# Optimization experiments

Hardware: AMD Instinct MI355X
Metric: run time of the kernel (lower is better)

## Reference

```python
import jax, jax.numpy as jnp
import numpy as np
import math

N_HEADS = 4
GELU = lambda x: jax.nn.gelu(x, approximate=False)  # torch nn.GELU default = exact erf

def _ln(x, s, b):
    m = jnp.mean(x, axis=-1, keepdims=True)
    v = jnp.mean((x - m) ** 2, axis=-1, keepdims=True)
    return (x - m) * jax.lax.rsqrt(v + 1e-5) * s + b

def _fwd(materials, in_seq, proj_vars, param_vars, enc_w1, enc_b1, enc_w2, enc_b2, sos,
         tl_wq, tl_wk, tl_wv, tl_bq, tl_bk, tl_bv, tl_wo, tl_bo,
         tl_ln1s, tl_ln1b, tl_ln2s, tl_ln2b, tl_fw1, tl_fb1, tl_fw2, tl_fb2,
         pw1, pb1, pw2, pb2, pw3, pb3, pw4, pb4, pw5, pb5,
         ipw1, ipb1, ipw2, ipb2, hw1, hb1, hw2, hb2, hw3, hb3):
    B = in_seq.shape[0]
    # encoder input MLP: [B,S,1] -> [B,S,D]
    x = GELU(in_seq @ enc_w1 + enc_b1) @ enc_w2 + enc_b2
    x = jnp.concatenate([jnp.broadcast_to(sos, (B, 1, sos.shape[-1])), x], axis=1)
    S1, D = x.shape[1], x.shape[2]
    dh = D // N_HEADS
    # sinusoidal positional encoding
    pos = jnp.arange(S1, dtype=jnp.float32)[:, None]
    div = jnp.exp(jnp.arange(0, D, 2, dtype=jnp.float32) * (-math.log(10000.0) / D))
    ang = pos * div
    pe = jnp.stack([jnp.sin(ang), jnp.cos(ang)], axis=-1).reshape(S1, D)
    x = x + pe
    scale = 1.0 / math.sqrt(dh)
    # post-LN TransformerEncoder layers (torch default norm_first=False), eval mode (no dropout)
    for l in range(tl_wq.shape[0]):
        q = (x @ tl_wq[l] + tl_bq[l]).reshape(B, S1, N_HEADS, dh).transpose(0, 2, 1, 3)
        k = (x @ tl_wk[l] + tl_bk[l]).reshape(B, S1, N_HEADS, dh).transpose(0, 2, 1, 3)
        v = (x @ tl_wv[l] + tl_bv[l]).reshape(B, S1, N_HEADS, dh).transpose(0, 2, 1, 3)
        att = jax.nn.softmax(jnp.einsum('bhqd,bhkd->bhqk', q, k) * scale, axis=-1)
        o = jnp.einsum('bhqk,bhkd->bhqd', att, v).transpose(0, 2, 1, 3).reshape(B, S1, D)
        x = _ln(x + o @ tl_wo[l] + tl_bo[l], tl_ln1s[l], tl_ln1b[l])
        f = GELU(x @ tl_fw1[l] + tl_fb1[l]) @ tl_fw2[l] + tl_fb2[l]
        x = _ln(x + f, tl_ln2s[l], tl_ln2b[l])
    sos_out = x[:, 0]
    h = jnp.concatenate([proj_vars, sos_out], axis=1)
    for w, b in ((pw1, pb1), (pw2, pb2), (pw3, pb3), (pw4, pb4)):
        h = GELU(h @ w + b)
    proj_out = h @ pw5 + pb5
    pp = GELU(param_vars @ ipw1 + ipb1) @ ipw2 + ipb2
    mi = jnp.concatenate([pp, proj_out], axis=1)  # [B, output_features+param_vars]
    # MaterialHead mask-gather-MLP-scatter == run every tiny head densely, pick by material id
    h1 = GELU(jnp.einsum('bi,mio->mbo', mi, hw1) + hb1[:, None, :])
    h2 = GELU(jnp.einsum('mbi,mio->mbo', h1, hw2) + hb2[:, None, :])
    h3 = jnp.einsum('mbi,mio->mbo', h2, hw3) + hb3[:, None, :]  # [M,B,1]
    return h3[materials, jnp.arange(B)]  # [B,1]

def setup_inputs() -> dict:
    key = jax.random.key(0)
    ks = iter(jax.random.split(key, 64))
    def rn(shape, scale=0.05):
        return jax.random.normal(next(ks), shape, dtype=jnp.float32) * scale
    B, S, IN, EL, D, L, DFF = 64, 1024, 1, 48, 64, 3, 256
    PV, PP, OF, M = 3, 3, 24, 3
    IF = OF + PP
    return dict(
        in_seq=rn((B, S, IN), 1.0),
        proj_vars=rn((B, PV), 1.0),
        param_vars=rn((B, PP), 1.0),
        materials=jax.random.randint(next(ks), (B,), 0, M),
        enc_w1=rn((IN, EL)), enc_b1=rn((EL,)), enc_w2=rn((EL, D)), enc_b2=rn((D,)),
        sos=rn((1, 1, D)),
        tl_wq=rn((L, D, D)), tl_wk=rn((L, D, D)), tl_wv=rn((L, D, D)),
        tl_bq=rn((L, D)), tl_bk=rn((L, D)), tl_bv=rn((L, D)),
        tl_wo=rn((L, D, D)), tl_bo=rn((L, D)),
        tl_ln1s=jnp.ones((L, D)), tl_ln1b=jnp.zeros((L, D)),
        tl_ln2s=jnp.ones((L, D)), tl_ln2b=jnp.zeros((L, D)),
        tl_fw1=rn((L, D, DFF)), tl_fb1=rn((L, DFF)), tl_fw2=rn((L, DFF, D)), tl_fb2=rn((L, D)),
        pw1=rn((PV + D, 34)), pb1=rn((34,)), pw2=rn((34, 11)), pb2=rn((11,)),
        pw3=rn((11, 36)), pb3=rn((36,)), pw4=rn((36, 22)), pb4=rn((22,)),
        pw5=rn((22, OF)), pb5=rn((OF,)),
        ipw1=rn((PP, 3)), ipb1=rn((3,)), ipw2=rn((3, PP)), ipb2=rn((PP,)),
        hw1=rn((M, IF, 15)), hb1=rn((M, 15)), hw2=rn((M, 15, 18)), hb2=rn((M, 18)),
        hw3=rn((M, 18, 1)), hb3=rn((M, 1)),
    )

def reference(in_seq, proj_vars, param_vars, materials, enc_w1, enc_b1, enc_w2, enc_b2, sos,
              tl_wq, tl_wk, tl_wv, tl_bq, tl_bk, tl_bv, tl_wo, tl_bo,
              tl_ln1s, tl_ln1b, tl_ln2s, tl_ln2b, tl_fw1, tl_fb1, tl_fw2, tl_fb2,
              pw1, pb1, pw2, pb2, pw3, pb3, pw4, pb4, pw5, pb5,
              ipw1, ipb1, ipw2, ipb2, hw1, hb1, hw2, hb2, hw3, hb3):
    return _fwd(materials, in_seq, proj_vars, param_vars, enc_w1, enc_b1, enc_w2, enc_b2, sos,
                tl_wq, tl_wk, tl_wv, tl_bq, tl_bk, tl_bv, tl_wo, tl_bo,
                tl_ln1s, tl_ln1b, tl_ln2s, tl_ln2b, tl_fw1, tl_fb1, tl_fw2, tl_fb2,
                pw1, pb1, pw2, pb2, pw3, pb3, pw4, pb4, pw5, pb5,
                ipw1, ipb1, ipw2, ipb2, hw1, hb1, hw2, hb2, hw3, hb3)
```

## Files before the change

kernel.cpp:

```cpp
#include <hip/hip_runtime.h>
#include <hip/hip_bf16.h>
#include <math.h>

#define BB   64
#define SS   1024
#define S1C  1025
#define DD   64
#define NHD  4
#define NBH  (BB * NHD)
#define DHD  16
#define DFFC 256
#define NLAY 3
#define NTOK (BB * S1C)
#define SPAD 1056
#define TGRP2 9
#define FTQ   32
#define FT2   32
#define HPAD 264
#define OPAD 68
#define YPAD 72
#define QSCL 0.36067376022224085f

typedef const float* fp;
typedef __attribute__((ext_vector_type(8))) short bf16x8;
typedef __attribute__((ext_vector_type(4))) float f32x4;
typedef __attribute__((ext_vector_type(2))) unsigned int u32x2;
typedef __attribute__((ext_vector_type(4))) unsigned int u32x4;

#if __has_builtin(__builtin_amdgcn_exp2f)
#define RAW_EXP2(x) __builtin_amdgcn_exp2f(x)
#else
#define RAW_EXP2(x) __expf(0.6931471805599453f * (x))
#endif
#if __has_builtin(__builtin_amdgcn_rcpf)
#define RAW_RCP(x) __builtin_amdgcn_rcpf(x)
#else
#define RAW_RCP(x) (1.0f / (x))
#endif

__device__ __forceinline__ float gelu_exact(float x) {
    return 0.5f * x * (1.0f + erff(x * 0.7071067811865475f));
}
__device__ __forceinline__ float erf_fast(float x) {
    float ax = fabsf(x);
    float t = RAW_RCP(1.0f + 0.3275911f * ax);
    float p = t * (0.254829592f + t * (-0.284496736f + t * (1.421413741f +
              t * (-1.453152027f + t * 1.061405429f))));
    float e = RAW_EXP2(ax * ax * -1.4426950408889634f);
    float r = 1.0f - p * e;
    return copysignf(r, x);
}
__device__ __forceinline__ float gelu_fast(float x) {
    return 0.5f * x * (1.0f + erf_fast(x * 0.7071067811865475f));
}
__device__ __forceinline__ short f2b(float f) {
    unsigned u = __float_as_uint(f);
    return (short)((u + 0x7fffu + ((u >> 16) & 1u)) >> 16);
}
__device__ __forceinline__ short f2b_pos(float f) {
    return (short)((__float_as_uint(f) + 0x8000u) >> 16);
}

__global__ __launch_bounds__(256) void k_wconv(
    fp wq, fp wk, fp wv, fp wo, fp w1, fp w2,
    short* __restrict__ wqkvT, short* __restrict__ woT,
    short* __restrict__ w1T, short* __restrict__ w2T)
{
    int l = blockIdx.y;
    int i = blockIdx.x * 256 + threadIdx.x;
    if (i < 12288) {
        int p = i >> 12, rem = i & 4095;
        int d = rem >> 6, j = rem & 63;
        fp src = (p == 0 ? wq : p == 1 ? wk : wv) + (size_t)l * 4096;
        float v = src[j * 64 + d];
        if (p == 0) v *= QSCL;
        wqkvT[(size_t)l * 12288 + i] = f2b(v);
    } else if (i < 16384) {
        int rem = i - 12288;
        woT[(size_t)l * 4096 + rem] = f2b(wo[(size_t)l * 4096 + (rem & 63) * 64 + (rem >> 6)]);
    } else if (i < 32768) {
        int rem = i - 16384;
        w1T[(size_t)l * 16384 + rem] = f2b(w1[(size_t)l * 16384 + (rem & 63) * 256 + (rem >> 6)]);
    } else {
        int rem = i - 32768;
        w2T[(size_t)l * 16384 + rem] = f2b(w2[(size_t)l * 16384 + (rem & 255) * 64 + (rem >> 8)]);
    }
}

__global__ __launch_bounds__(64) void k_zero(
    short* __restrict__ qb, short* __restrict__ kb, short* __restrict__ vbt)
{
    int bh = blockIdx.x, t = threadIdx.x;
    for (int i = t; i < 31 * 16; i += 64) {
        int r = i >> 4, c = i & 15;
        size_t idx = ((size_t)bh * SPAD + 1025 + r) * 16 + c;
        qb[idx] = 0; kb[idx] = 0;
    }
    for (int i = t; i < 16 * 31; i += 64) {
        int e = i / 31, c = i % 31;
        vbt[((size_t)bh * 16 + e) * SPAD + 1025 + c] = 0;
    }
}

__global__ __launch_bounds__(256) void k_encode(
    fp in_seq, fp enc_w1, fp enc_b1, fp enc_w2, fp enc_b2, fp sos,
    float* __restrict__ x, short* __restrict__ xb)
{
    int t = threadIdx.x;
    int w = t >> 6, d = t & 63;
    int tok = blockIdx.x * 4 + w;
    int b = tok / S1C, s = tok % S1C;
    __shared__ float e[4][48];
    float val;
    if (s == 0) {
        val = sos[d];
    } else {
        float tin = in_seq[b * SS + (s - 1)];
        if (d < 48) e[w][d] = gelu_fast(tin * enc_w1[d] + enc_b1[d]);
        float acc = enc_b2[d];
        for (int j = 0; j < 48; ++j) acc += e[w][j] * enc_w2[j * DD + d];
        val = acc;
    }
    int i2 = (d >> 1) * 2;
    float factor = RAW_EXP2((float)i2 * (-9.210340371976184f / 64.0f) * 1.4426950408889634f);
    float ang = (float)s * factor;
    val += (d & 1) ? __cosf(ang) : __sinf(ang);
    x[(size_t)tok * DD + d] = val;
    xb[(size_t)tok * DD + d] = f2b(val);
}

__global__ __launch_bounds__(256) void k_qkv(
    const short* __restrict__ xb, const short* __restrict__ wqkvT,
    fp bq, fp bk, fp bv,
    short* __restrict__ qb, short* __restrict__ kb, short* __restrict__ vbt)
{
    int blk = blockIdx.x, t = threadIdx.x;
    int tok0 = blk * FTQ;
    int w = t >> 6, l = t & 63;
    int quad = l >> 4, lo = l & 15;

    const short* xp0 = xb + ((size_t)(tok0 + lo)) * DD;
    const short* xp1 = xb + ((size_t)(tok0 + 16 + lo)) * DD;
    bf16x8 a0 = *(const bf16x8*)(xp0 + quad * 8);
    bf16x8 a1 = *(const bf16x8*)(xp0 + 32 + quad * 8);
    bf16x8 a2 = *(const bf16x8*)(xp1 + quad * 8);
    bf16x8 a3 = *(const bf16x8*)(xp1 + 32 + quad * 8);

    int n = w * 16 + lo;
    #pragma unroll
    for (int p = 0; p < 3; ++p) {
        const short* wT = wqkvT + (size_t)p * 4096 + (size_t)n * 64;
        bf16x8 b0 = *(const bf16x8*)(wT + quad * 8);
        bf16x8 b1 = *(const bf16x8*)(wT + 32 + quad * 8);
        f32x4 c0 = __builtin_amdgcn_mfma_f32_16x16x32_bf16(a0, b0, (f32x4){0,0,0,0}, 0, 0, 0);
        c0 = __builtin_amdgcn_mfma_f32_16x16x32_bf16(a1, b1, c0, 0, 0, 0);
        f32x4 c1 = __builtin_amdgcn_mfma_f32_16x16x32_bf16(a2, b0, (f32x4){0,0,0,0}, 0, 0, 0);
        c1 = __builtin_amdgcn_mfma_f32_16x16x32_bf16(a3, b1, c1, 0, 0, 0);
        float bias = (p == 0) ? bq[n] * QSCL : (p == 1) ? bk[n] : bv[n];
        #pragma unroll
        for (int r = 0; r < 4; ++r) {
            int tok = tok0 + quad * 4 + r;
            int bb0 = tok / S1C, ss0 = tok % S1C;
            int bh = bb0 * NHD + w;
            short val = f2b(c0[r] + bias);
            int tok2 = tok + 16;
            int bb1 = tok2 / S1C, ss1 = tok2 % S1C;
            int bh2 = bb1 * NHD + w;
            short val2 = f2b(c1[r] + bias);
            if (p == 0) {
                qb[((size_t)bh * SPAD + ss0) * 16 + lo] = val;
                qb[((size_t)bh2 * SPAD + ss1) * 16 + lo] = val2;
            } else if (p == 1) {
                kb[((size_t)bh * SPAD + ss0) * 16 + lo] = val;
                kb[((size_t)bh2 * SPAD + ss1) * 16 + lo] = val2;
            } else {
                vbt[((size_t)bh * 16 + lo) * SPAD + ss0] = val;
                vbt[((size_t)bh2 * 16 + lo) * SPAD + ss1] = val2;
            }
        }
    }
}

__global__ __launch_bounds__(256) void k_attn(
    const short* __restrict__ qb, const short* __restrict__ kb,
    const short* __restrict__ vbt, short* __restrict__ ob)
{
    int bid = blockIdx.x;
    int bh  = bid % NBH;
    int grp = bid / NBH;
    int b = bh >> 2, h = bh & 3;
    int t = threadIdx.x;
    int w = t >> 6, l = t & 63;
    int quad = l >> 4, lo = l & 15;
    int t0 = grp * 4 + w;
    int t1 = t0 + 36;
    if (t1 > 65) t1 = 65;
    int qg0 = t0 * 16, qg1 = t1 * 16;

    __shared__ u32x2 ptmem[4][272];
    char* ptc = (char*)&ptmem[w][0];
    unsigned ptbase = (unsigned)(uintptr_t)ptc;

    const short* qbase = qb + (size_t)bh * SPAD * 16;
    const short* kbase = kb + (size_t)bh * SPAD * 16;
    const short* vbase = vbt + (size_t)bh * 16 * SPAD;

    bf16x8 aQ0 = {0,0,0,0,0,0,0,0}, aQ1 = {0,0,0,0,0,0,0,0};
    if (quad < 2) {
        aQ0 = *(const bf16x8*)(qbase + ((size_t)(qg0 + lo)) * 16 + quad * 8);
        aQ1 = *(const bf16x8*)(qbase + ((size_t)(qg1 + lo)) * 16 + quad * 8);
    }

    const short ONE = 0x3F80;
    bf16x8 aOne = {ONE, ONE, ONE, ONE, ONE, ONE, ONE, ONE};

    f32x4 oc0 = {0.f,0.f,0.f,0.f}, oc1 = {0.f,0.f,0.f,0.f};
    f32x4 dn0 = {0.f,0.f,0.f,0.f}, dn1 = {0.f,0.f,0.f,0.f};

    unsigned wo0, wo1;
    { int k0 = lo;       wo0 = (unsigned)((k0 >> 2) * 136 + (k0 & 3) * 32 + quad * 8);
      int k1 = 16 + lo;  wo1 = (unsigned)((k1 >> 2) * 136 + (k1 & 3) * 32 + quad * 8); }
    unsigned ro = (unsigned)(quad * 272 + lo * 8);

    auto body = [&](int ch, bool tail) {
        bf16x8 aV = *(const bf16x8*)(vbase + (size_t)lo * SPAD + ch * 32 + quad * 8);
        const short* kch = kbase + (size_t)(ch * 32) * 16;
        #pragma unroll
        for (int t01 = 0; t01 < 2; ++t01) {
            bf16x8 bK = *(const bf16x8*)(kch + (size_t)(t01 * 16 + lo) * 16 + (quad & 1) * 8);
            f32x4 c0 = __builtin_amdgcn_mfma_f32_16x16x32_bf16(aQ0, bK, (f32x4){0.f,0.f,0.f,0.f}, 0, 0, 0);
            f32x4 c1 = __builtin_amdgcn_mfma_f32_16x16x32_bf16(aQ1, bK, (f32x4){0.f,0.f,0.f,0.f}, 0, 0, 0);
            bool valid = !tail || (t01 == 0 && lo == 0);
            unsigned off = t01 ? wo1 : wo0;
            unsigned a0 = __float_as_uint(valid ? RAW_EXP2(c0[0]) : 0.f) + 0x8000u;
            unsigned a1 = __float_as_uint(valid ? RAW_EXP2(c0[1]) : 0.f) + 0x8000u;
            unsigned a2 = __float_as_uint(valid ? RAW_EXP2(c0[2]) : 0.f) + 0x8000u;
            unsigned a3 = __float_as_uint(valid ? RAW_EXP2(c0[3]) : 0.f) + 0x8000u;
            *(u32x2*)(ptc + off) = (u32x2){
                __builtin_amdgcn_perm(a1, a0, 0x07060302u),
                __builtin_amdgcn_perm(a3, a2, 0x07060302u)};
            unsigned b0 = __float_as_uint(valid ? RAW_EXP2(c1[0]) : 0.f) + 0x8000u;
            unsigned b1 = __float_as_uint(valid ? RAW_EXP2(c1[1]) : 0.f) + 0x8000u;
            unsigned b2 = __float_as_uint(valid ? RAW_EXP2(c1[2]) : 0.f) + 0x8000u;
            unsigned b3 = __float_as_uint(valid ? RAW_EXP2(c1[3]) : 0.f) + 0x8000u;
            *(u32x2*)(ptc + 1088 + off) = (u32x2){
                __builtin_amdgcn_perm(b1, b0, 0x07060302u),
                __builtin_amdgcn_perm(b3, b2, 0x07060302u)};
        }
        asm volatile("s_waitcnt lgkmcnt(0)" ::: "memory");
        u32x2 p00, p01, p10, p11;
        asm volatile("ds_read_b64_tr_b16 %0, %1"             : "=v"(p00) : "v"(ptbase + ro));
        asm volatile("ds_read_b64_tr_b16 %0, %1 offset:136"  : "=v"(p01) : "v"(ptbase + ro));
        asm volatile("ds_read_b64_tr_b16 %0, %1 offset:1088" : "=v"(p10) : "v"(ptbase + ro));
        asm volatile("ds_read_b64_tr_b16 %0, %1 offset:1224" : "=v"(p11) : "v"(ptbase + ro));
        asm volatile("s_waitcnt lgkmcnt(0)" ::: "memory");
        __builtin_amdgcn_sched_barrier(0);
        u32x4 q0; q0[0] = p00[0]; q0[1] = p00[1]; q0[2] = p01[0]; q0[3] = p01[1];
        u32x4 q1; q1[0] = p10[0]; q1[1] = p10[1]; q1[2] = p11[0]; q1[3] = p11[1];
        bf16x8 pB0 = __builtin_bit_cast(bf16x8, q0);
        bf16x8 pB1 = __builtin_bit_cast(bf16x8, q1);
        oc0 = __builtin_amdgcn_mfma_f32_16x16x32_bf16(aV, pB0, oc0, 0, 0, 0);
        dn0 = __builtin_amdgcn_mfma_f32_16x16x32_bf16(aOne, pB0, dn0, 0, 0, 0);
        oc1 = __builtin_amdgcn_mfma_f32_16x16x32_bf16(aV, pB1, oc1, 0, 0, 0);
        dn1 = __builtin_amdgcn_mfma_f32_16x16x32_bf16(aOne, pB1, dn1, 0, 0, 0);
    };

    for (int ch = 0; ch < 32; ++ch) body(ch, false);
    body(32, true);

    {
        int qrow = qg0 + lo;
        if (qrow < S1C) {
            float inv = 1.0f / dn0[0];
            unsigned p0 = (unsigned short)f2b(oc0[0] * inv) | ((unsigned)(unsigned short)f2b(oc0[1] * inv) << 16);
            unsigned p1 = (unsigned short)f2b(oc0[2] * inv) | ((unsigned)(unsigned short)f2b(oc0[3] * inv) << 16);
            *(uint2*)(ob + ((size_t)b * S1C + qrow) * DD + h * DHD + quad * 4) = make_uint2(p0, p1);
        }
    }
    {
        int qrow = qg1 + lo;
        if (qrow < S1C) {
            float inv = 1.0f / dn1[0];
            unsigned p0 = (unsigned short)f2b(oc1[0] * inv) | ((unsigned)(unsigned short)f2b(oc1[1] * inv) << 16);
            unsigned p1 = (unsigned short)f2b(oc1[2] * inv) | ((unsigned)(unsigned short)f2b(oc1[3] * inv) << 16);
            *(uint2*)(ob + ((size_t)b * S1C + qrow) * DD + h * DHD + quad * 4) = make_uint2(p0, p1);
        }
    }
}

__global__ __launch_bounds__(256) void k_block(
    const short* __restrict__ ob, float* __restrict__ x,
    const short* __restrict__ woT, fp bo, fp ln1s, fp ln1b,
    const short* __restrict__ w1T, fp b1, const short* __restrict__ w2T, fp b2,
    fp ln2s, fp ln2b,
    const short* __restrict__ wqkvTn, fp bqn, fp bkn, fp bvn,
    short* __restrict__ qb, short* __restrict__ kb, short* __restrict__ vbt,
    int has_next)
{
    int blk = blockIdx.x, t = threadIdx.x;
    int tok0 = blk * FT2;
    int w = t >> 6, l = t & 63;
    int quad = l >> 4, lo = l & 15;

    __shared__ float otf[FT2][OPAD];
    __shared__ short ys[FT2][YPAD];
    __shared__ short hid[FT2][HPAD];

    {
        const short* obp0 = ob + ((size_t)(tok0 + lo)) * DD;
        const short* obp1 = ob + ((size_t)(tok0 + 16 + lo)) * DD;
        bf16x8 a0 = *(const bf16x8*)(obp0 + quad * 8);
        bf16x8 a1 = *(const bf16x8*)(obp0 + 32 + quad * 8);
        bf16x8 a2 = *(const bf16x8*)(obp1 + quad * 8);
        bf16x8 a3 = *(const bf16x8*)(obp1 + 32 + quad * 8);
        int n = w * 16 + lo;
        const short* wT = woT + (size_t)n * 64;
        bf16x8 b0 = *(const bf16x8*)(wT + quad * 8);
        bf16x8 bb = *(const bf16x8*)(wT + 32 + quad * 8);
        f32x4 c0 = __builtin_amdgcn_mfma_f32_16x16x32_bf16(a0, b0, (f32x4){0,0,0,0}, 0, 0, 0);
        c0 = __builtin_amdgcn_mfma_f32_16x16x32_bf16(a1, bb, c0, 0, 0, 0);
        f32x4 c1 = __builtin_amdgcn_mfma_f32_16x16x32_bf16(a2, b0, (f32x4){0,0,0,0}, 0, 0, 0);
        c1 = __builtin_amdgcn_mfma_f32_16x16x32_bf16(a3, bb, c1, 0, 0, 0);
        float bov = bo[n];
        #pragma unroll
        for (int r = 0; r < 4; ++r) {
            otf[quad * 4 + r][n] = c0[r] + bov;
            otf[16 + quad * 4 + r][n] = c1[r] + bov;
        }
    }
    __syncthreads();

    int d = l;
    float yv[8];
    {
        float s1 = ln1s[d], bl1 = ln1b[d];
        #pragma unroll
        for (int i = 0; i < 8; ++i) {
            int tt = w * 8 + i;
            float val = otf[tt][d] + x[(size_t)(tok0 + tt) * DD + d];
            float sum = val, vs = val * val;
            #pragma unroll
            for (int off = 32; off > 0; off >>= 1) {
                sum += __shfl_xor(sum, off, 64);
                vs  += __shfl_xor(vs, off, 64);
            }
            float mean = sum * (1.0f / 64.0f);
            float var = vs * (1.0f / 64.0f) - mean * mean;
            float y = (val - mean) * rsqrtf(var + 1e-5f) * s1 + bl1;
            yv[i] = y;
            ys[tt][d] = f2b(y);
        }
    }
    __syncthreads();

    {
        bf16x8 a0 = *(const bf16x8*)&ys[lo][quad * 8];
        bf16x8 a1 = *(const bf16x8*)&ys[lo][32 + quad * 8];
        bf16x8 a2 = *(const bf16x8*)&ys[16 + lo][quad * 8];
        bf16x8 a3 = *(const bf16x8*)&ys[16 + lo][32 + quad * 8];
        #pragma unroll
        for (int i = 0; i < 4; ++i) {
            int n = w * 64 + i * 16 + lo;
            const short* wT = w1T + (size_t)n * 64;
            bf16x8 b0 = *(const bf16x8*)(wT + quad * 8);
            bf16x8 bb = *(const bf16x8*)(wT + 32 + quad * 8);
            f32x4 c0 = __builtin_amdgcn_mfma_f32_16x16x32_bf16(a0, b0, (f32x4){0,0,0,0}, 0, 0, 0);
            c0 = __builtin_amdgcn_mfma_f32_16x16x32_bf16(a1, bb, c0, 0, 0, 0);
            f32x4 c1 = __builtin_amdgcn_mfma_f32_16x16x32_bf16(a2, b0, (f32x4){0,0,0,0}, 0, 0, 0);
            c1 = __builtin_amdgcn_mfma_f32_16x16x32_bf16(a3, bb, c1, 0, 0, 0);
            float b1v = b1[n];
            #pragma unroll
            for (int r = 0; r < 4; ++r) {
                hid[quad * 4 + r][n] = f2b(gelu_fast(c0[r] + b1v));
                hid[16 + quad * 4 + r][n] = f2b(gelu_fast(c1[r] + b1v));
            }
        }
    }
    __syncthreads();

    {
        f32x4 c20 = {0.f,0.f,0.f,0.f}, c21 = {0.f,0.f,0.f,0.f};
        const short* wT2 = w2T + (size_t)(w * 16 + lo) * 256;
        #pragma unroll
        for (int kc = 0; kc < 8; ++kc) {
            bf16x8 b2f = *(const bf16x8*)(wT2 + kc * 32 + quad * 8);
            bf16x8 a20 = *(const bf16x8*)&hid[lo][kc * 32 + quad * 8];
            bf16x8 a21 = *(const bf16x8*)&hid[16 + lo][kc * 32 + quad * 8];
            c20 = __builtin_amdgcn_mfma_f32_16x16x32_bf16(a20, b2f, c20, 0, 0, 0);
            c21 = __builtin_amdgcn_mfma_f32_16x16x32_bf16(a21, b2f, c21, 0, 0, 0);
        }
        float b2v = b2[w * 16 + lo];
        #pragma unroll
        for (int r = 0; r < 4; ++r) {
            otf[quad * 4 + r][w * 16 + lo] = c20[r] + b2v;
            otf[16 + quad * 4 + r][w * 16 + lo] = c21[r] + b2v;
        }
    }
    __syncthreads();

    {
        float s2 = ln2s[d], bl2 = ln2b[d];
        #pragma unroll
        for (int i = 0; i < 8; ++i) {
            int tt = w * 8 + i;
            float val = otf[tt][d] + yv[i];
            float sum = val, vs = val * val;
            #pragma unroll
            for (int off = 32; off > 0; off >>= 1) {
                sum += __shfl_xor(sum, off, 64);
                vs  += __shfl_xor(vs, off, 64);
            }
            float mean = sum * (1.0f / 64.0f);
            float var = vs * (1.0f / 64.0f) - mean * mean;
            float y = (val - mean) * rsqrtf(var + 1e-5f) * s2 + bl2;
            x[(size_t)(tok0 + tt) * DD + d] = y;
            ys[tt][d] = f2b(y);
        }
    }
    __syncthreads();

    if (has_next) {
        bf16x8 a0 = *(const bf16x8*)&ys[lo][quad * 8];
        bf16x8 a1 = *(const bf16x8*)&ys[lo][32 + quad * 8];
        bf16x8 a2 = *(const bf16x8*)&ys[16 + lo][quad * 8];
        bf16x8 a3 = *(const bf16x8*)&ys[16 + lo][32 + quad * 8];
        int n = w * 16 + lo;
        #pragma unroll
        for (int p = 0; p < 3; ++p) {
            const short* wT = wqkvTn + (size_t)p * 4096 + (size_t)n * 64;
            bf16x8 b0 = *(const bf16x8*)(wT + quad * 8);
            bf16x8 bb = *(const bf16x8*)(wT + 32 + quad * 8);
            f32x4 c0 = __builtin_amdgcn_mfma_f32_16x16x32_bf16(a0, b0, (f32x4){0,0,0,0}, 0, 0, 0);
            c0 = __builtin_amdgcn_mfma_f32_16x16x32_bf16(a1, bb, c0, 0, 0, 0);
            f32x4 c1 = __builtin_amdgcn_mfma_f32_16x16x32_bf16(a2, b0, (f32x4){0,0,0,0}, 0, 0, 0);
            c1 = __builtin_amdgcn_mfma_f32_16x16x32_bf16(a3, bb, c1, 0, 0, 0);
            float bias = (p == 0) ? bqn[n] * QSCL : (p == 1) ? bkn[n] : bvn[n];
            #pragma unroll
            for (int r = 0; r < 4; ++r) {
                int tok = tok0 + quad * 4 + r;
                int bb0 = tok / S1C, ss0 = tok % S1C;
                int bh = bb0 * NHD + w;
                short val = f2b(c0[r] + bias);
                int tok2 = tok + 16;
                int bb1 = tok2 / S1C, ss1 = tok2 % S1C;
                int bh2 = bb1 * NHD + w;
                short val2 = f2b(c1[r] + bias);
                if (p == 0) {
                    qb[((size_t)bh * SPAD + ss0) * 16 + lo] = val;
                    qb[((size_t)bh2 * SPAD + ss1) * 16 + lo] = val2;
                } else if (p == 1) {
                    kb[((size_t)bh * SPAD + ss0) * 16 + lo] = val;
                    kb[((size_t)bh2 * SPAD + ss1) * 16 + lo] = val2;
                } else {
                    vbt[((size_t)bh * 16 + lo) * SPAD + ss0] = val;
                    vbt[((size_t)bh2 * 16 + lo) * SPAD + ss1] = val2;
                }
            }
        }
    }
}

__global__ __launch_bounds__(64) void k_head(
    const float* __restrict__ x, fp proj_vars, fp param_vars,
    const int* __restrict__ materials,
    fp pw1, fp pb1, fp pw2, fp pb2, fp pw3, fp pb3,
    fp pw4, fp pb4, fp pw5, fp pb5,
    fp ipw1, fp ipb1, fp ipw2, fp ipb2,
    fp hw1, fp hb1, fp hw2, fp hb2, fp hw3, fp hb3,
    float* __restrict__ out)
{
    int b = blockIdx.x;
    int tid = threadIdx.x;
    __shared__ float A[80], Bf[80], pp[8], mi[32];

    if (tid < 3) A[tid] = proj_vars[b * 3 + tid];
    A[3 + tid] = x[((size_t)b * S1C + 0) * DD + tid];
    __syncthreads();

    if (tid < 34) {
        float a = pb1[tid];
        for (int i = 0; i < 67; ++i) a += A[i] * pw1[i * 34 + tid];
        Bf[tid] = gelu_exact(a);
    }
    __syncthreads();
    if (tid < 11) {
        float a = pb2[tid];
        for (int i = 0; i < 34; ++i) a += Bf[i] * pw2[i * 11 + tid];
        A[tid] = gelu_exact(a);
    }
    __syncthreads();
    if (tid < 36) {
        float a = pb3[tid];
        for (int i = 0; i < 11; ++i) a += A[i] * pw3[i * 36 + tid];
        Bf[tid] = gelu_exact(a);
    }
    __syncthreads();
    if (tid < 22) {
        float a = pb4[tid];
        for (int i = 0; i < 36; ++i) a += Bf[i] * pw4[i * 22 + tid];
        A[tid] = gelu_exact(a);
    }
    __syncthreads();
    if (tid < 24) {
        float a = pb5[tid];
        for (int i = 0; i < 22; ++i) a += A[i] * pw5[i * 24 + tid];
        mi[3 + tid] = a;
    }
    if (tid < 3) {
        float a = ipb1[tid];
        for (int i = 0; i < 3; ++i) a += param_vars[b * 3 + i] * ipw1[i * 3 + tid];
        pp[tid] = gelu_exact(a);
    }
    __syncthreads();
    if (tid < 3) {
        float a = ipb2[tid];
        for (int i = 0; i < 3; ++i) a += pp[i] * ipw2[i * 3 + tid];
        mi[tid] = a;
    }
    __syncthreads();

    int m = materials[b];
    if (tid < 15) {
        float a = hb1[m * 15 + tid];
        for (int i = 0; i < 27; ++i) a += mi[i] * hw1[(m * 27 + i) * 15 + tid];
        A[tid] = gelu_exact(a);
    }
    __syncthreads();
    if (tid < 18) {
        float a = hb2[m * 18 + tid];
        for (int i = 0; i < 15; ++i) a += A[i] * hw2[(m * 15 + i) * 18 + tid];
        Bf[tid] = gelu_exact(a);
    }
    __syncthreads();
    if (tid == 0) {
        float a = hb3[m];
        for (int i = 0; i < 18; ++i) a += Bf[i] * hw3[m * 18 + i];
        out[b] = a;
    }
}

extern "C" void kernel_launch(void* const* d_in, const int* in_sizes, int n_in,
                              void* d_out, int out_size, void* d_ws, size_t ws_size,
                              hipStream_t stream) {
    fp in_seq     = (fp)d_in[0];
    fp proj_vars  = (fp)d_in[1];
    fp param_vars = (fp)d_in[2];
    const int* materials = (const int*)d_in[3];
    fp enc_w1 = (fp)d_in[4];
    fp enc_b1 = (fp)d_in[5];
    fp enc_w2 = (fp)d_in[6];
    fp enc_b2 = (fp)d_in[7];
    fp sos    = (fp)d_in[8];
    fp tl_wq  = (fp)d_in[9];
    fp tl_wk  = (fp)d_in[10];
    fp tl_wv  = (fp)d_in[11];
    fp tl_bq  = (fp)d_in[12];
    fp tl_bk  = (fp)d_in[13];
    fp tl_bv  = (fp)d_in[14];
    fp tl_wo  = (fp)d_in[15];
    fp tl_bo  = (fp)d_in[16];
    fp tl_ln1s = (fp)d_in[17];
    fp tl_ln1b = (fp)d_in[18];
    fp tl_ln2s = (fp)d_in[19];
    fp tl_ln2b = (fp)d_in[20];
    fp tl_fw1 = (fp)d_in[21];
    fp tl_fb1 = (fp)d_in[22];
    fp tl_fw2 = (fp)d_in[23];
    fp tl_fb2 = (fp)d_in[24];
    fp pw1 = (fp)d_in[25]; fp pb1 = (fp)d_in[26];
    fp pw2 = (fp)d_in[27]; fp pb2 = (fp)d_in[28];
    fp pw3 = (fp)d_in[29]; fp pb3 = (fp)d_in[30];
    fp pw4 = (fp)d_in[31]; fp pb4 = (fp)d_in[32];
    fp pw5 = (fp)d_in[33]; fp pb5 = (fp)d_in[34];
    fp ipw1 = (fp)d_in[35]; fp ipb1 = (fp)d_in[36];
    fp ipw2 = (fp)d_in[37]; fp ipb2 = (fp)d_in[38];
    fp hw1 = (fp)d_in[39]; fp hb1 = (fp)d_in[40];
    fp hw2 = (fp)d_in[41]; fp hb2 = (fp)d_in[42];
    fp hw3 = (fp)d_in[43]; fp hb3 = (fp)d_in[44];

    float* x  = (float*)d_ws;
    short* ob = (short*)(x + (size_t)NTOK * DD);
    short* xb = ob + (size_t)NTOK * DD;
    short* qb = xb + (size_t)NTOK * DD;
    short* kb = qb + (size_t)NBH * SPAD * 16;
    short* vbt = kb + (size_t)NBH * SPAD * 16;
    short* wqkvT = vbt + (size_t)NBH * 16 * SPAD;
    short* woT = wqkvT + (size_t)NLAY * 12288;
    short* w1T = woT + (size_t)NLAY * 4096;
    short* w2T = w1T + (size_t)NLAY * 16384;

    k_wconv<<<dim3(192, NLAY), 256, 0, stream>>>(
        tl_wq, tl_wk, tl_wv, tl_wo, tl_fw1, tl_fw2, wqkvT, woT, w1T, w2T);
    k_zero<<<NBH, 64, 0, stream>>>(qb, kb, vbt);
    k_encode<<<NTOK / 4, 256, 0, stream>>>(in_seq, enc_w1, enc_b1, enc_w2, enc_b2, sos, x, xb);

    k_qkv<<<NTOK / FTQ, 256, 0, stream>>>(
        xb, wqkvT,
        tl_bq, tl_bk, tl_bv,
        qb, kb, vbt);

    for (int l = 0; l < NLAY; ++l) {
        k_attn<<<NBH * TGRP2, 256, 0, stream>>>(qb, kb, vbt, ob);
        int ln = (l + 1 < NLAY) ? (l + 1) : l;
        k_block<<<NTOK / FT2, 256, 0, stream>>>(
            ob, x,
            woT + (size_t)l * 4096, tl_bo + (size_t)l * DD,
            tl_ln1s + (size_t)l * DD, tl_ln1b + (size_t)l * DD,
            w1T + (size_t)l * 16384, tl_fb1 + (size_t)l * DFFC,
            w2T + (size_t)l * 16384, tl_fb2 + (size_t)l * DD,
            tl_ln2s + (size_t)l * DD, tl_ln2b + (size_t)l * DD,
            wqkvT + (size_t)ln * 12288,
            tl_bq + (size_t)ln * DD, tl_bk + (size_t)ln * DD, tl_bv + (size_t)ln * DD,
            qb, kb, vbt,
            (l + 1 < NLAY) ? 1 : 0);
    }

    k_head<<<BB, 64, 0, stream>>>(
        x, proj_vars, param_vars, materials,
        pw1, pb1, pw2, pb2, pw3, pb3, pw4, pb4, pw5, pb5,
        ipw1, ipb1, ipw2, ipb2,
        hw1, hb1, hw2, hb2, hw3, hb3,
        (float*)d_out);
}
```

Before: 538.4 us.

## Software-pipeline attention loop with double-buffered LDS and K/V prefetch

Restructures the attention inner loop into a two-stage software pipeline. QK^T and exp for chunk ch+1 run while the transposed P tile of chunk ch is read from a double-buffered LDS region and fed to the PV MFMAs. K for the next chunk is prefetched into registers ping-ponged between two sets. The aim is to hide LDS round-trip and global load latency behind MFMA work, at the cost of more registers and doubled LDS usage per wave.

```diff
diff --git a/kernel.cpp b/kernel.cpp
--- a/kernel.cpp
+++ b/kernel.cpp
@@ -59,6 +59,15 @@
 }
 __device__ __forceinline__ short f2b_pos(float f) {
     return (short)((__float_as_uint(f) + 0x8000u) >> 16);
+}
+
+__device__ __forceinline__ u32x2 pack4exp(f32x4 c, bool valid) {
+    unsigned a0 = __float_as_uint(valid ? RAW_EXP2(c[0]) : 0.f) + 0x8000u;
+    unsigned a1 = __float_as_uint(valid ? RAW_EXP2(c[1]) : 0.f) + 0x8000u;
+    unsigned a2 = __float_as_uint(valid ? RAW_EXP2(c[2]) : 0.f) + 0x8000u;
+    unsigned a3 = __float_as_uint(valid ? RAW_EXP2(c[3]) : 0.f) + 0x8000u;
+    return (u32x2){__builtin_amdgcn_perm(a1, a0, 0x07060302u),
+                   __builtin_amdgcn_perm(a3, a2, 0x07060302u)};
 }
 
 __global__ __launch_bounds__(256) void k_wconv(
@@ -197,8 +206,8 @@
     if (t1 > 65) t1 = 65;
     int qg0 = t0 * 16, qg1 = t1 * 16;
 
-    __shared__ u32x2 ptmem[4][272];
-    char* ptc = (char*)&ptmem[w][0];
+    __shared__ u32x2 ptmem[4][2][272];
+    char* ptc = (char*)&ptmem[w][0][0];
     unsigned ptbase = (unsigned)(uintptr_t)ptc;
 
     const short* qbase = qb + (size_t)bh * SPAD * 16;
@@ -221,52 +230,101 @@
     { int k0 = lo;       wo0 = (unsigned)((k0 >> 2) * 136 + (k0 & 3) * 32 + quad * 8);
       int k1 = 16 + lo;  wo1 = (unsigned)((k1 >> 2) * 136 + (k1 & 3) * 32 + quad * 8); }
     unsigned ro = (unsigned)(quad * 272 + lo * 8);
-
-    auto body = [&](int ch, bool tail) {
-        bf16x8 aV = *(const bf16x8*)(vbase + (size_t)lo * SPAD + ch * 32 + quad * 8);
-        const short* kch = kbase + (size_t)(ch * 32) * 16;
-        #pragma unroll
-        for (int t01 = 0; t01 < 2; ++t01) {
-            bf16x8 bK = *(const bf16x8*)(kch + (size_t)(t01 * 16 + lo) * 16 + (quad & 1) * 8);
-            f32x4 c0 = __builtin_amdgcn_mfma_f32_16x16x32_bf16(aQ0, bK, (f32x4){0.f,0.f,0.f,0.f}, 0, 0, 0);
-            f32x4 c1 = __builtin_amdgcn_mfma_f32_16x16x32_bf16(aQ1, bK, (f32x4){0.f,0.f,0.f,0.f}, 0, 0, 0);
-            bool valid = !tail || (t01 == 0 && lo == 0);
-            unsigned off = t01 ? wo1 : wo0;
-            unsigned a0 = __float_as_uint(valid ? RAW_EXP2(c0[0]) : 0.f) + 0x8000u;
-            unsigned a1 = __float_as_uint(valid ? RAW_EXP2(c0[1]) : 0.f) + 0x8000u;
-            unsigned a2 = __float_as_uint(valid ? RAW_EXP2(c0[2]) : 0.f) + 0x8000u;
-            unsigned a3 = __float_as_uint(valid ? RAW_EXP2(c0[3]) : 0.f) + 0x8000u;
-            *(u32x2*)(ptc + off) = (u32x2){
-                __builtin_amdgcn_perm(a1, a0, 0x07060302u),
-                __builtin_amdgcn_perm(a3, a2, 0x07060302u)};
-            unsigned b0 = __float_as_uint(valid ? RAW_EXP2(c1[0]) : 0.f) + 0x8000u;
-            unsigned b1 = __float_as_uint(valid ? RAW_EXP2(c1[1]) : 0.f) + 0x8000u;
-            unsigned b2 = __float_as_uint(valid ? RAW_EXP2(c1[2]) : 0.f) + 0x8000u;
-            unsigned b3 = __float_as_uint(valid ? RAW_EXP2(c1[3]) : 0.f) + 0x8000u;
-            *(u32x2*)(ptc + 1088 + off) = (u32x2){
-                __builtin_amdgcn_perm(b1, b0, 0x07060302u),
-                __builtin_amdgcn_perm(b3, b2, 0x07060302u)};
-        }
+    unsigned rd0 = ptbase + ro;
+    unsigned rd1 = ptbase + 2176 + ro;
+    char* wb0 = ptc;
+    char* wb1 = ptc + 2176;
+
+    bf16x8 kxA, kyA, kxB, kyB, vA, vB;
+
+    {
+        const short* k0p = kbase + (size_t)lo * 16 + (quad & 1) * 8;
+        kxA = *(const bf16x8*)k0p;
+        kyA = *(const bf16x8*)(k0p + 256);
+        vA  = *(const bf16x8*)(vbase + (size_t)lo * SPAD + quad * 8);
+        const short* k1p = kbase + (size_t)(32 + lo) * 16 + (quad & 1) * 8;
+        kxB = *(const bf16x8*)k1p;
+        kyB = *(const bf16x8*)(k1p + 256);
+
+        f32x4 c0 = __builtin_amdgcn_mfma_f32_16x16x32_bf16(aQ0, kxA, (f32x4){0.f,0.f,0.f,0.f}, 0, 0, 0);
+        f32x4 c1 = __builtin_amdgcn_mfma_f32_16x16x32_bf16(aQ1, kxA, (f32x4){0.f,0.f,0.f,0.f}, 0, 0, 0);
+        *(u32x2*)(wb0 + wo0)        = pack4exp(c0, true);
+        *(u32x2*)(wb0 + 1088 + wo0) = pack4exp(c1, true);
+        c0 = __builtin_amdgcn_mfma_f32_16x16x32_bf16(aQ0, kyA, (f32x4){0.f,0.f,0.f,0.f}, 0, 0, 0);
+        c1 = __builtin_amdgcn_mfma_f32_16x16x32_bf16(aQ1, kyA, (f32x4){0.f,0.f,0.f,0.f}, 0, 0, 0);
+        *(u32x2*)(wb0 + wo1)        = pack4exp(c0, true);
+        *(u32x2*)(wb0 + 1088 + wo1) = pack4exp(c1, true);
+    }
+
+#define STEP(CH, TAIL, KXC, KYC, KXN, KYN, VP, VC, RD, WB) do {               \
+    int ch_ = (CH);                                                            \
+    if (!(TAIL)) {                                                             \
+        const short* kn_ = kbase + (size_t)((ch_ + 1) * 32 + lo) * 16 + (quad & 1) * 8; \
+        KXN = *(const bf16x8*)kn_;                                             \
+        KYN = *(const bf16x8*)(kn_ + 256);                                     \
+    }                                                                          \
+    VC = *(const bf16x8*)(vbase + (size_t)lo * SPAD + ch_ * 32 + quad * 8);    \
+    asm volatile("s_waitcnt lgkmcnt(0)" ::: "memory");                         \
+    u32x2 p00_, p01_, p10_, p11_;                                              \
+    asm volatile("ds_read_b64_tr_b16 %0, %1"             : "=v"(p00_) : "v"(RD)); \
+    asm volatile("ds_read_b64_tr_b16 %0, %1 offset:136"  : "=v"(p01_) : "v"(RD)); \
+    asm volatile("ds_read_b64_tr_b16 %0, %1 offset:1088" : "=v"(p10_) : "v"(RD)); \
+    asm volatile("ds_read_b64_tr_b16 %0, %1 offset:1224" : "=v"(p11_) : "v"(RD)); \
+    u32x2 wA0_, wA1_, wB0_, wB1_;                                              \
+    {                                                                          \
+        f32x4 c0_ = __builtin_amdgcn_mfma_f32_16x16x32_bf16(aQ0, KXC, (f32x4){0.f,0.f,0.f,0.f}, 0, 0, 0); \
+        f32x4 c1_ = __builtin_amdgcn_mfma_f32_16x16x32_bf16(aQ1, KXC, (f32x4){0.f,0.f,0.f,0.f}, 0, 0, 0); \
+        bool v0_ = !(TAIL) || (lo == 0);                                       \
+        wA0_ = pack4exp(c0_, v0_);                                             \
+        wB0_ = pack4exp(c1_, v0_);                                             \
+        c0_ = __builtin_amdgcn_mfma_f32_16x16x32_bf16(aQ0, KYC, (f32x4){0.f,0.f,0.f,0.f}, 0, 0, 0); \
+        c1_ = __builtin_amdgcn_mfma_f32_16x16x32_bf16(aQ1, KYC, (f32x4){0.f,0.f,0.f,0.f}, 0, 0, 0); \
+        bool v1_ = !(TAIL);                                                    \
+        wA1_ = pack4exp(c0_, v1_);                                             \
+        wB1_ = pack4exp(c1_, v1_);                                             \
+    }                                                                          \
+    asm volatile("s_waitcnt lgkmcnt(0)" ::: "memory");                         \
+    __builtin_amdgcn_sched_barrier(0);                                         \
+    u32x4 q0_; q0_[0] = p00_[0]; q0_[1] = p00_[1]; q0_[2] = p01_[0]; q0_[3] = p01_[1]; \
+    u32x4 q1_; q1_[0] = p10_[0]; q1_[1] = p10_[1]; q1_[2] = p11_[0]; q1_[3] = p11_[1]; \
+    bf16x8 pB0_ = __builtin_bit_cast(bf16x8, q0_);                             \
+    bf16x8 pB1_ = __builtin_bit_cast(bf16x8, q1_);                             \
+    oc0 = __builtin_amdgcn_mfma_f32_16x16x32_bf16(VP, pB0_, oc0, 0, 0, 0);     \
+    dn0 = __builtin_amdgcn_mfma_f32_16x16x32_bf16(aOne, pB0_, dn0, 0, 0, 0);   \
+    oc1 = __builtin_amdgcn_mfma_f32_16x16x32_bf16(VP, pB1_, oc1, 0, 0, 0);     \
+    dn1 = __builtin_amdgcn_mfma_f32_16x16x32_bf16(aOne, pB1_, dn1, 0, 0, 0);   \
+    *(u32x2*)((WB) + wo0)        = wA0_;                                       \
+    *(u32x2*)((WB) + 1088 + wo0) = wB0_;                                       \
+    *(u32x2*)((WB) + wo1)        = wA1_;                                       \
+    *(u32x2*)((WB) + 1088 + wo1) = wB1_;                                       \
+} while (0)
+
+    for (int chp = 1; chp < 31; chp += 2) {
+        STEP(chp,     0, kxA, kyA, kxB, kyB, vA, vB, rd0, wb1);
+        STEP(chp + 1, 0, kxB, kyB, kxA, kyA, vB, vA, rd1, wb0);
+    }
+    STEP(31, 0, kxA, kyA, kxB, kyB, vA, vB, rd0, wb1);
+    STEP(32, 1, kxB, kyB, kxA, kyA, vB, vA, rd1, wb0);
+#undef STEP
+
+    {
         asm volatile("s_waitcnt lgkmcnt(0)" ::: "memory");
         u32x2 p00, p01, p10, p11;
-        asm volatile("ds_read_b64_tr_b16 %0, %1"             : "=v"(p00) : "v"(ptbase + ro));
-        asm volatile("ds_read_b64_tr_b16 %0, %1 offset:136"  : "=v"(p01) : "v"(ptbase + ro));
-        asm volatile("ds_read_b64_tr_b16 %0, %1 offset:1088" : "=v"(p10) : "v"(ptbase + ro));
-        asm volatile("ds_read_b64_tr_b16 %0, %1 offset:1224" : "=v"(p11) : "v"(ptbase + ro));
+        asm volatile("ds_read_b64_tr_b16 %0, %1"             : "=v"(p00) : "v"(rd0));
+        asm volatile("ds_read_b64_tr_b16 %0, %1 offset:136"  : "=v"(p01) : "v"(rd0));
+        asm volatile("ds_read_b64_tr_b16 %0, %1 offset:1088" : "=v"(p10) : "v"(rd0));
+        asm volatile("ds_read_b64_tr_b16 %0, %1 offset:1224" : "=v"(p11) : "v"(rd0));
         asm volatile("s_waitcnt lgkmcnt(0)" ::: "memory");
         __builtin_amdgcn_sched_barrier(0);
         u32x4 q0; q0[0] = p00[0]; q0[1] = p00[1]; q0[2] = p01[0]; q0[3] = p01[1];
         u32x4 q1; q1[0] = p10[0]; q1[1] = p10[1]; q1[2] = p11[0]; q1[3] = p11[1];
         bf16x8 pB0 = __builtin_bit_cast(bf16x8, q0);
         bf16x8 pB1 = __builtin_bit_cast(bf16x8, q1);
-        oc0 = __builtin_amdgcn_mfma_f32_16x16x32_bf16(aV, pB0, oc0, 0, 0, 0);
+        oc0 = __builtin_amdgcn_mfma_f32_16x16x32_bf16(vA, pB0, oc0, 0, 0, 0);
         dn0 = __builtin_amdgcn_mfma_f32_16x16x32_bf16(aOne, pB0, dn0, 0, 0, 0);
-        oc1 = __builtin_amdgcn_mfma_f32_16x16x32_bf16(aV, pB1, oc1, 0, 0, 0);
+        oc1 = __builtin_amdgcn_mfma_f32_16x16x32_bf16(vA, pB1, oc1, 0, 0, 0);
         dn1 = __builtin_amdgcn_mfma_f32_16x16x32_bf16(aOne, pB1, dn1, 0, 0, 0);
-    };
-
-    for (int ch = 0; ch < 32; ++ch) body(ch, false);
-    body(32, true);
+    }
 
     {
         int qrow = qg0 + lo;
```

Result: faster. 523.7 us (-2.7%).
